# Kernel tuning notes

Hardware: AMD Instinct MI355X
Metric: run time of the kernel (lower is better)

The kernel has to match this reference:

```python
import jax, jax.numpy as jnp
import numpy as np

NORM_EPS = 1e-8   # eps in F.normalize
PDIST_EPS = 1e-6  # eps in nn.PairwiseDistance(2, eps=1e-06): ||x1 - x2 + eps||_2


def setup_inputs() -> dict:
    key = jax.random.key(0)
    student_output = jax.random.normal(key, (16384, 1024), dtype=jnp.float32)
    return {"student_output": student_output}


def reference(student_output) -> jnp.ndarray:
    x = student_output
    n = x.shape[0]
    # --- pairwise NN via inner products on L2-normalized vectors (no-grad in original) ---
    norms = jnp.linalg.norm(x, axis=-1, keepdims=True)
    xn = x / jnp.maximum(norms, NORM_EPS)          # F.normalize(x, p=2, eps=1e-8)
    dots = xn @ xn.T                               # [N, N]
    dots = dots.at[jnp.diag_indices(n)].set(-1.0)  # mask self-similarity
    I = jnp.argmax(dots, axis=1)                   # nearest neighbor indices
    # --- pairwise L2 distance to NN (torch adds eps to the difference) ---
    diff = x - x[I] + PDIST_EPS                    # [N, D]
    distances = jnp.sqrt(jnp.sum(diff * diff, axis=-1))
    loss = -jnp.mean(jnp.log(distances))
    return loss
```

## Files before the change

### kernel.cpp

```cpp
#include <hip/hip_runtime.h>
#include <hip/hip_bf16.h>

#define KN 16384
#define KD 1024
#define NB (KN / 128)

typedef __attribute__((ext_vector_type(4))) int   i32x4;
typedef __attribute__((ext_vector_type(8))) int   i32x8;
typedef __attribute__((ext_vector_type(4))) float f32x4;
typedef __attribute__((ext_vector_type(2))) unsigned int u32x2;

#define SCALE_M6 0x79797979
#define FMT_FP4  4

__device__ __forceinline__ i32x8 ldg_frag4(const unsigned char* p) {
  const i32x4 v = *(const i32x4*)p;
  return __builtin_shufflevector(v, v, 0, 1, 2, 3, -1, -1, -1, -1);
}

#define IDX_MASK 0x3FFFu
#define VAL_MASK 0xFFFFC000u

__device__ __forceinline__ unsigned fp4n(float x) {
  const float a = fabsf(x);
  unsigned c = (unsigned)(a >= 0.25f) + (unsigned)(a >= 0.75f)
             + (unsigned)(a >= 1.25f) + (unsigned)(a >= 1.75f)
             + (unsigned)(a >= 2.5f)  + (unsigned)(a >= 3.5f)
             + (unsigned)(a >= 5.0f);
  return c | ((__float_as_uint(x) >> 28) & 8u);
}

#if defined(__has_builtin)
#if __has_builtin(__builtin_amdgcn_cvt_scalef32_pk_fp4_f32)
#define HW_FP4 1
#endif
#endif

__global__ __launch_bounds__(256) void k_normalize(const float* __restrict__ x,
                                                   unsigned char* __restrict__ xn,
                                                   unsigned* __restrict__ best) {
  const int lane = threadIdx.x & 63;
  const int wave = threadIdx.x >> 6;
  const int row  = (blockIdx.x << 2) + wave;
  if (lane == 0) best[row] = 0u;
  const float4* xr = (const float4*)(x + (size_t)row * KD);
  const float4 v0 = xr[(lane << 2) + 0];
  const float4 v1 = xr[(lane << 2) + 1];
  const float4 v2 = xr[(lane << 2) + 2];
  const float4 v3 = xr[(lane << 2) + 3];
  float ss = v0.x * v0.x + v0.y * v0.y + v0.z * v0.z + v0.w * v0.w
           + v1.x * v1.x + v1.y * v1.y + v1.z * v1.z + v1.w * v1.w
           + v2.x * v2.x + v2.y * v2.y + v2.z * v2.z + v2.w * v2.w
           + v3.x * v3.x + v3.y * v3.y + v3.z * v3.z + v3.w * v3.w;
#pragma unroll
  for (int off = 32; off > 0; off >>= 1) ss += __shfl_xor(ss, off);
  const float scale = 64.0f / fmaxf(sqrtf(ss), 1e-8f);
  const float s0  = v0.x * scale, s1  = v0.y * scale, s2  = v0.z * scale, s3  = v0.w * scale;
  const float s4  = v1.x * scale, s5  = v1.y * scale, s6  = v1.z * scale, s7  = v1.w * scale;
  const float s8  = v2.x * scale, s9  = v2.y * scale, s10 = v2.z * scale, s11 = v2.w * scale;
  const float s12 = v3.x * scale, s13 = v3.y * scale, s14 = v3.z * scale, s15 = v3.w * scale;
  unsigned w0 = 0u, w1 = 0u;
#ifdef HW_FP4
  w0 = __builtin_amdgcn_cvt_scalef32_pk_fp4_f32(w0, s0,  s1,  1.0f, 0);
  w0 = __builtin_amdgcn_cvt_scalef32_pk_fp4_f32(w0, s2,  s3,  1.0f, 1);
  w0 = __builtin_amdgcn_cvt_scalef32_pk_fp4_f32(w0, s4,  s5,  1.0f, 2);
  w0 = __builtin_amdgcn_cvt_scalef32_pk_fp4_f32(w0, s6,  s7,  1.0f, 3);
  w1 = __builtin_amdgcn_cvt_scalef32_pk_fp4_f32(w1, s8,  s9,  1.0f, 0);
  w1 = __builtin_amdgcn_cvt_scalef32_pk_fp4_f32(w1, s10, s11, 1.0f, 1);
  w1 = __builtin_amdgcn_cvt_scalef32_pk_fp4_f32(w1, s12, s13, 1.0f, 2);
  w1 = __builtin_amdgcn_cvt_scalef32_pk_fp4_f32(w1, s14, s15, 1.0f, 3);
#else
  w0 = (fp4n(s0)  | (fp4n(s1)  << 4)) | ((fp4n(s2)  | (fp4n(s3)  << 4)) << 8)
     | ((fp4n(s4) | (fp4n(s5)  << 4)) << 16) | ((fp4n(s6)  | (fp4n(s7)  << 4)) << 24);
  w1 = (fp4n(s8)  | (fp4n(s9)  << 4)) | ((fp4n(s10) | (fp4n(s11) << 4)) << 8)
     | ((fp4n(s12)| (fp4n(s13) << 4)) << 16) | ((fp4n(s14) | (fp4n(s15) << 4)) << 24);
#endif
  unsigned char* base = xn + ((size_t)(row >> 4) << 13) + ((size_t)(lane >> 3) << 10)
                      + ((((lane & 6) << 3) + (row & 15)) << 4) + ((lane & 1) << 3);
  *(u32x2*)base = (u32x2){w0, w1};
}

template <bool DIAG>
__device__ __forceinline__ void epilogue(const f32x4 (&acc)[4][4], int by, int bx,
                                         int wm, int wn, int quad, int l15,
                                         unsigned* __restrict__ best) {
  const int rowbase = (by << 7) + wm * 64 + (quad << 2);
  const int colbase = (bx << 7) + wn * 64 + l15;
  unsigned cm0 = 0u, cm1 = 0u, cm2 = 0u, cm3 = 0u;
#pragma unroll
  for (int i = 0; i < 4; i++) {
#pragma unroll
    for (int r = 0; r < 4; r++) {
      const int grow = rowbase + i * 16 + r;
      const unsigned grx = (unsigned)grow ^ IDX_MASK;
      unsigned rm = 0u;
#pragma unroll
      for (int j = 0; j < 4; j++) {
        const int gcol = colbase + j * 16;
        unsigned t = (__float_as_uint(fmaf(acc[i][j][r], 0.125f, 3.0f)) << 9) & VAL_MASK;
        if (DIAG && gcol == grow) t = 0u;
        const unsigned rc = t | ((unsigned)gcol ^ IDX_MASK);
        const unsigned cc = t | grx;
        rm = rm > rc ? rm : rc;
        if (j == 0) cm0 = cm0 > cc ? cm0 : cc;
        if (j == 1) cm1 = cm1 > cc ? cm1 : cc;
        if (j == 2) cm2 = cm2 > cc ? cm2 : cc;
        if (j == 3) cm3 = cm3 > cc ? cm3 : cc;
      }
#pragma unroll
      for (int off = 1; off < 16; off <<= 1) {
        const unsigned o = __shfl_xor(rm, off);
        rm = rm > o ? rm : o;
      }
      if (l15 == 0) atomicMax(best + grow, rm);
    }
  }
  if (!DIAG) {
    unsigned cm[4] = {cm0, cm1, cm2, cm3};
#pragma unroll
    for (int j = 0; j < 4; j++) {
      unsigned o = __shfl_xor(cm[j], 16);
      cm[j] = cm[j] > o ? cm[j] : o;
      o = __shfl_xor(cm[j], 32);
      cm[j] = cm[j] > o ? cm[j] : o;
      if (quad == 0) atomicMax(best + colbase + j * 16, cm[j]);
    }
  }
}

__global__ __launch_bounds__(256, 2) void k_nn_argmax(const unsigned char* __restrict__ xn,
                                                      unsigned* __restrict__ best) {
  const int id = blockIdx.x;
  int d, by;
  if (id < 8192) {
    const int o   = id & 7;
    const int idp = id >> 3;
    const int k   = idp >> 6;
    const int p   = idp & 63;
    const int q   = o + (k << 3);
    by = ((q & 15) << 3) + (p & 7);
    d  = ((q >> 4) << 3) + (p >> 3);
  } else {
    d  = NB / 2;
    by = id - 8192;
  }
  const int bx = (by + d) & (NB - 1);

  const int tid  = threadIdx.x;
  const int lane = tid & 63;
  const int wave = tid >> 6;
  const int wm   = wave >> 1;
  const int wn   = wave & 1;
  const int quad = lane >> 4;
  const int l15  = lane & 15;

  f32x4 acc[4][4];
#pragma unroll
  for (int i = 0; i < 4; i++)
#pragma unroll
    for (int j = 0; j < 4; j++) acc[i][j] = (f32x4){0.f, 0.f, 0.f, 0.f};

  const unsigned char* pa = xn + ((size_t)((by << 3) + (wm << 2)) << 13) + (lane << 4);
  const unsigned char* pb = xn + ((size_t)((bx << 3) + (wn << 2)) << 13) + (lane << 4);

#pragma unroll 2
  for (int kb = 0; kb < 8; kb++) {
    const int ko = kb << 10;
    const i32x8 a0 = ldg_frag4(pa + ko);
    const i32x8 a1 = ldg_frag4(pa + (1 << 13) + ko);
    const i32x8 a2 = ldg_frag4(pa + (2 << 13) + ko);
    const i32x8 a3 = ldg_frag4(pa + (3 << 13) + ko);
    const i32x8 b0 = ldg_frag4(pb + ko);
    const i32x8 b1 = ldg_frag4(pb + (1 << 13) + ko);
    const i32x8 b2 = ldg_frag4(pb + (2 << 13) + ko);
    const i32x8 b3 = ldg_frag4(pb + (3 << 13) + ko);
    acc[0][0] = __builtin_amdgcn_mfma_scale_f32_16x16x128_f8f6f4(a0, b0, acc[0][0], FMT_FP4, FMT_FP4, 0, SCALE_M6, 0, SCALE_M6);
    acc[1][0] = __builtin_amdgcn_mfma_scale_f32_16x16x128_f8f6f4(a1, b0, acc[1][0], FMT_FP4, FMT_FP4, 0, SCALE_M6, 0, SCALE_M6);
    acc[2][0] = __builtin_amdgcn_mfma_scale_f32_16x16x128_f8f6f4(a2, b0, acc[2][0], FMT_FP4, FMT_FP4, 0, SCALE_M6, 0, SCALE_M6);
    acc[3][0] = __builtin_amdgcn_mfma_scale_f32_16x16x128_f8f6f4(a3, b0, acc[3][0], FMT_FP4, FMT_FP4, 0, SCALE_M6, 0, SCALE_M6);
    acc[0][1] = __builtin_amdgcn_mfma_scale_f32_16x16x128_f8f6f4(a0, b1, acc[0][1], FMT_FP4, FMT_FP4, 0, SCALE_M6, 0, SCALE_M6);
    acc[1][1] = __builtin_amdgcn_mfma_scale_f32_16x16x128_f8f6f4(a1, b1, acc[1][1], FMT_FP4, FMT_FP4, 0, SCALE_M6, 0, SCALE_M6);
    acc[2][1] = __builtin_amdgcn_mfma_scale_f32_16x16x128_f8f6f4(a2, b1, acc[2][1], FMT_FP4, FMT_FP4, 0, SCALE_M6, 0, SCALE_M6);
    acc[3][1] = __builtin_amdgcn_mfma_scale_f32_16x16x128_f8f6f4(a3, b1, acc[3][1], FMT_FP4, FMT_FP4, 0, SCALE_M6, 0, SCALE_M6);
    acc[0][2] = __builtin_amdgcn_mfma_scale_f32_16x16x128_f8f6f4(a0, b2, acc[0][2], FMT_FP4, FMT_FP4, 0, SCALE_M6, 0, SCALE_M6);
    acc[1][2] = __builtin_amdgcn_mfma_scale_f32_16x16x128_f8f6f4(a1, b2, acc[1][2], FMT_FP4, FMT_FP4, 0, SCALE_M6, 0, SCALE_M6);
    acc[2][2] = __builtin_amdgcn_mfma_scale_f32_16x16x128_f8f6f4(a2, b2, acc[2][2], FMT_FP4, FMT_FP4, 0, SCALE_M6, 0, SCALE_M6);
    acc[3][2] = __builtin_amdgcn_mfma_scale_f32_16x16x128_f8f6f4(a3, b2, acc[3][2], FMT_FP4, FMT_FP4, 0, SCALE_M6, 0, SCALE_M6);
    acc[0][3] = __builtin_amdgcn_mfma_scale_f32_16x16x128_f8f6f4(a0, b3, acc[0][3], FMT_FP4, FMT_FP4, 0, SCALE_M6, 0, SCALE_M6);
    acc[1][3] = __builtin_amdgcn_mfma_scale_f32_16x16x128_f8f6f4(a1, b3, acc[1][3], FMT_FP4, FMT_FP4, 0, SCALE_M6, 0, SCALE_M6);
    acc[2][3] = __builtin_amdgcn_mfma_scale_f32_16x16x128_f8f6f4(a2, b3, acc[2][3], FMT_FP4, FMT_FP4, 0, SCALE_M6, 0, SCALE_M6);
    acc[3][3] = __builtin_amdgcn_mfma_scale_f32_16x16x128_f8f6f4(a3, b3, acc[3][3], FMT_FP4, FMT_FP4, 0, SCALE_M6, 0, SCALE_M6);
  }

  if (d == 0) epilogue<true>(acc, by, bx, wm, wn, quad, l15, best);
  else        epilogue<false>(acc, by, bx, wm, wn, quad, l15, best);
}

__global__ __launch_bounds__(256) void k_dist(const float* __restrict__ x,
                                              const unsigned* __restrict__ best,
                                              float* __restrict__ rowlog) {
  const int lane = threadIdx.x & 63;
  const int wave = threadIdx.x >> 6;
  const int row  = (blockIdx.x << 2) + wave;
  const int nb   = (int)((~best[row]) & IDX_MASK);
  const float4* ar = (const float4*)(x + (size_t)row * KD);
  const float4* br = (const float4*)(x + (size_t)nb * KD);
  float ss = 0.f;
#pragma unroll
  for (int q = 0; q < 4; q++) {
    const float4 a = ar[lane + 64 * q];
    const float4 b = br[lane + 64 * q];
    const float dx = a.x - b.x + 1e-6f;
    const float dy = a.y - b.y + 1e-6f;
    const float dz = a.z - b.z + 1e-6f;
    const float dw = a.w - b.w + 1e-6f;
    ss += dx * dx + dy * dy + dz * dz + dw * dw;
  }
#pragma unroll
  for (int off = 32; off > 0; off >>= 1) ss += __shfl_xor(ss, off);
  if (lane == 0) rowlog[row] = -logf(sqrtf(ss));
}

__global__ __launch_bounds__(1024) void k_final(const float* __restrict__ rowlog,
                                                float* __restrict__ out) {
  const int tid = threadIdx.x;
  float s = 0.f;
  for (int i = tid; i < KN; i += 1024) s += rowlog[i];
#pragma unroll
  for (int off = 32; off > 0; off >>= 1) s += __shfl_down(s, off);
  __shared__ float ws[16];
  if ((tid & 63) == 0) ws[tid >> 6] = s;
  __syncthreads();
  if (tid == 0) {
    float t = 0.f;
#pragma unroll
    for (int i = 0; i < 16; i++) t += ws[i];
    out[0] = t / (float)KN;
  }
}

extern "C" void kernel_launch(void* const* d_in, const int* in_sizes, int n_in,
                              void* d_out, int out_size, void* d_ws, size_t ws_size,
                              hipStream_t stream) {
  const float* x = (const float*)d_in[0];
  float* out = (float*)d_out;

  char* ws = (char*)d_ws;
  unsigned char* xn = (unsigned char*)ws;
  unsigned* best = (unsigned*)(ws + (size_t)KN * KD / 2);
  float* rowlog = (float*)(ws + (size_t)KN * KD / 2 + (size_t)KN * 4);

  k_normalize<<<KN / 4, 256, 0, stream>>>(x, xn, best);
  k_nn_argmax<<<8192 + 64, 256, 0, stream>>>(xn, best);
  k_dist<<<KN / 4, 256, 0, stream>>>(x, best, rowlog);
  k_final<<<1, 1024, 0, stream>>>(rowlog, out);
}
```

Before: 221.6 us.

## Switch NN argmax GEMM to 32x32x64 FP4 MFMA with matching epilogue

Replaces the 4x4 grid of 16x16x128 scaled FP4 MFMAs per wave with a 2x2 grid of 32x32x64 MFMAs, remapping lane offsets into the existing packed FP4 layout and iterating 16 K-steps instead of 8. The epilogue is rewritten for the 32x32 accumulator layout, reducing rows across 32 lanes and columns across the two half-waves. The goal is fewer MFMA issues and fragment loads per K step, and fewer atomics per wave. It relies on the new lane-to-address mapping matching the 32x32x64 operand layout exactly.

```diff
diff --git a/kernel.cpp b/kernel.cpp
--- a/kernel.cpp
+++ b/kernel.cpp
@@ -5,10 +5,10 @@
 #define KD 1024
 #define NB (KN / 128)
 
-typedef __attribute__((ext_vector_type(4))) int   i32x4;
-typedef __attribute__((ext_vector_type(8))) int   i32x8;
-typedef __attribute__((ext_vector_type(4))) float f32x4;
-typedef __attribute__((ext_vector_type(2))) unsigned int u32x2;
+typedef __attribute__((ext_vector_type(4)))  int   i32x4;
+typedef __attribute__((ext_vector_type(8)))  int   i32x8;
+typedef __attribute__((ext_vector_type(16))) float f32x16;
+typedef __attribute__((ext_vector_type(2)))  unsigned int u32x2;
 
 #define SCALE_M6 0x79797979
 #define FMT_FP4  4
@@ -81,49 +81,46 @@
 }
 
 template <bool DIAG>
-__device__ __forceinline__ void epilogue(const f32x4 (&acc)[4][4], int by, int bx,
-                                         int wm, int wn, int quad, int l15,
-                                         unsigned* __restrict__ best) {
-  const int rowbase = (by << 7) + wm * 64 + (quad << 2);
-  const int colbase = (bx << 7) + wn * 64 + l15;
-  unsigned cm0 = 0u, cm1 = 0u, cm2 = 0u, cm3 = 0u;
-#pragma unroll
-  for (int i = 0; i < 4; i++) {
-#pragma unroll
-    for (int r = 0; r < 4; r++) {
-      const int grow = rowbase + i * 16 + r;
+__device__ __forceinline__ void epilogue32(const f32x16 (&acc)[2][2], int by, int bx,
+                                           int wm, int wn, int l31, int hi,
+                                           unsigned* __restrict__ best) {
+  const int rowbase = (by << 7) + wm * 64 + (hi << 2);
+  const int colbase = (bx << 7) + wn * 64 + l31;
+  unsigned cm0 = 0u, cm1 = 0u;
+#pragma unroll
+  for (int m = 0; m < 2; m++) {
+#pragma unroll
+    for (int reg = 0; reg < 16; reg++) {
+      const int grow = rowbase + m * 32 + (reg & 3) + ((reg >> 2) << 3);
       const unsigned grx = (unsigned)grow ^ IDX_MASK;
       unsigned rm = 0u;
 #pragma unroll
-      for (int j = 0; j < 4; j++) {
-        const int gcol = colbase + j * 16;
-        unsigned t = (__float_as_uint(fmaf(acc[i][j][r], 0.125f, 3.0f)) << 9) & VAL_MASK;
+      for (int n = 0; n < 2; n++) {
+        const int gcol = colbase + n * 32;
+        unsigned t = (__float_as_uint(fmaf(acc[m][n][reg], 0.125f, 3.0f)) << 9) & VAL_MASK;
         if (DIAG && gcol == grow) t = 0u;
         const unsigned rc = t | ((unsigned)gcol ^ IDX_MASK);
         const unsigned cc = t | grx;
         rm = rm > rc ? rm : rc;
-        if (j == 0) cm0 = cm0 > cc ? cm0 : cc;
-        if (j == 1) cm1 = cm1 > cc ? cm1 : cc;
-        if (j == 2) cm2 = cm2 > cc ? cm2 : cc;
-        if (j == 3) cm3 = cm3 > cc ? cm3 : cc;
+        if (n == 0) cm0 = cm0 > cc ? cm0 : cc;
+        else        cm1 = cm1 > cc ? cm1 : cc;
       }
 #pragma unroll
-      for (int off = 1; off < 16; off <<= 1) {
+      for (int off = 1; off < 32; off <<= 1) {
         const unsigned o = __shfl_xor(rm, off);
         rm = rm > o ? rm : o;
       }
-      if (l15 == 0) atomicMax(best + grow, rm);
+      if (l31 == 0) atomicMax(best + grow, rm);
     }
   }
   if (!DIAG) {
-    unsigned cm[4] = {cm0, cm1, cm2, cm3};
-#pragma unroll
-    for (int j = 0; j < 4; j++) {
-      unsigned o = __shfl_xor(cm[j], 16);
-      cm[j] = cm[j] > o ? cm[j] : o;
-      o = __shfl_xor(cm[j], 32);
-      cm[j] = cm[j] > o ? cm[j] : o;
-      if (quad == 0) atomicMax(best + colbase + j * 16, cm[j]);
+    unsigned o = __shfl_xor(cm0, 32);
+    cm0 = cm0 > o ? cm0 : o;
+    o = __shfl_xor(cm1, 32);
+    cm1 = cm1 > o ? cm1 : o;
+    if (hi == 0) {
+      atomicMax(best + colbase, cm0);
+      atomicMax(best + colbase + 32, cm1);
     }
   }
 }
@@ -151,49 +148,38 @@
   const int wave = tid >> 6;
   const int wm   = wave >> 1;
   const int wn   = wave & 1;
-  const int quad = lane >> 4;
-  const int l15  = lane & 15;
-
-  f32x4 acc[4][4];
-#pragma unroll
-  for (int i = 0; i < 4; i++)
-#pragma unroll
-    for (int j = 0; j < 4; j++) acc[i][j] = (f32x4){0.f, 0.f, 0.f, 0.f};
-
-  const unsigned char* pa = xn + ((size_t)((by << 3) + (wm << 2)) << 13) + (lane << 4);
-  const unsigned char* pb = xn + ((size_t)((bx << 3) + (wn << 2)) << 13) + (lane << 4);
-
-#pragma unroll 2
-  for (int kb = 0; kb < 8; kb++) {
-    const int ko = kb << 10;
-    const i32x8 a0 = ldg_frag4(pa + ko);
-    const i32x8 a1 = ldg_frag4(pa + (1 << 13) + ko);
-    const i32x8 a2 = ldg_frag4(pa + (2 << 13) + ko);
-    const i32x8 a3 = ldg_frag4(pa + (3 << 13) + ko);
-    const i32x8 b0 = ldg_frag4(pb + ko);
-    const i32x8 b1 = ldg_frag4(pb + (1 << 13) + ko);
-    const i32x8 b2 = ldg_frag4(pb + (2 << 13) + ko);
-    const i32x8 b3 = ldg_frag4(pb + (3 << 13) + ko);
-    acc[0][0] = __builtin_amdgcn_mfma_scale_f32_16x16x128_f8f6f4(a0, b0, acc[0][0], FMT_FP4, FMT_FP4, 0, SCALE_M6, 0, SCALE_M6);
-    acc[1][0] = __builtin_amdgcn_mfma_scale_f32_16x16x128_f8f6f4(a1, b0, acc[1][0], FMT_FP4, FMT_FP4, 0, SCALE_M6, 0, SCALE_M6);
-    acc[2][0] = __builtin_amdgcn_mfma_scale_f32_16x16x128_f8f6f4(a2, b0, acc[2][0], FMT_FP4, FMT_FP4, 0, SCALE_M6, 0, SCALE_M6);
-    acc[3][0] = __builtin_amdgcn_mfma_scale_f32_16x16x128_f8f6f4(a3, b0, acc[3][0], FMT_FP4, FMT_FP4, 0, SCALE_M6, 0, SCALE_M6);
-    acc[0][1] = __builtin_amdgcn_mfma_scale_f32_16x16x128_f8f6f4(a0, b1, acc[0][1], FMT_FP4, FMT_FP4, 0, SCALE_M6, 0, SCALE_M6);
-    acc[1][1] = __builtin_amdgcn_mfma_scale_f32_16x16x128_f8f6f4(a1, b1, acc[1][1], FMT_FP4, FMT_FP4, 0, SCALE_M6, 0, SCALE_M6);
-    acc[2][1] = __builtin_amdgcn_mfma_scale_f32_16x16x128_f8f6f4(a2, b1, acc[2][1], FMT_FP4, FMT_FP4, 0, SCALE_M6, 0, SCALE_M6);
-    acc[3][1] = __builtin_amdgcn_mfma_scale_f32_16x16x128_f8f6f4(a3, b1, acc[3][1], FMT_FP4, FMT_FP4, 0, SCALE_M6, 0, SCALE_M6);
-    acc[0][2] = __builtin_amdgcn_mfma_scale_f32_16x16x128_f8f6f4(a0, b2, acc[0][2], FMT_FP4, FMT_FP4, 0, SCALE_M6, 0, SCALE_M6);
-    acc[1][2] = __builtin_amdgcn_mfma_scale_f32_16x16x128_f8f6f4(a1, b2, acc[1][2], FMT_FP4, FMT_FP4, 0, SCALE_M6, 0, SCALE_M6);
-    acc[2][2] = __builtin_amdgcn_mfma_scale_f32_16x16x128_f8f6f4(a2, b2, acc[2][2], FMT_FP4, FMT_FP4, 0, SCALE_M6, 0, SCALE_M6);
-    acc[3][2] = __builtin_amdgcn_mfma_scale_f32_16x16x128_f8f6f4(a3, b2, acc[3][2], FMT_FP4, FMT_FP4, 0, SCALE_M6, 0, SCALE_M6);
-    acc[0][3] = __builtin_amdgcn_mfma_scale_f32_16x16x128_f8f6f4(a0, b3, acc[0][3], FMT_FP4, FMT_FP4, 0, SCALE_M6, 0, SCALE_M6);
-    acc[1][3] = __builtin_amdgcn_mfma_scale_f32_16x16x128_f8f6f4(a1, b3, acc[1][3], FMT_FP4, FMT_FP4, 0, SCALE_M6, 0, SCALE_M6);
-    acc[2][3] = __builtin_amdgcn_mfma_scale_f32_16x16x128_f8f6f4(a2, b3, acc[2][3], FMT_FP4, FMT_FP4, 0, SCALE_M6, 0, SCALE_M6);
-    acc[3][3] = __builtin_amdgcn_mfma_scale_f32_16x16x128_f8f6f4(a3, b3, acc[3][3], FMT_FP4, FMT_FP4, 0, SCALE_M6, 0, SCALE_M6);
-  }
-
-  if (d == 0) epilogue<true>(acc, by, bx, wm, wn, quad, l15, best);
-  else        epilogue<false>(acc, by, bx, wm, wn, quad, l15, best);
+  const int l31  = lane & 31;
+  const int hi   = lane >> 5;
+
+  f32x16 acc[2][2];
+#pragma unroll
+  for (int m = 0; m < 2; m++)
+#pragma unroll
+    for (int n = 0; n < 2; n++)
+#pragma unroll
+      for (int r = 0; r < 16; r++) acc[m][n][r] = 0.f;
+
+  const int lofs = (((lane >> 4) & 1) << 13) + (hi << 8) + ((lane & 15) << 4);
+  const unsigned char* pa0 = xn + ((size_t)((by << 3) + (wm << 2)) << 13) + lofs;
+  const unsigned char* pa1 = pa0 + 16384;
+  const unsigned char* pb0 = xn + ((size_t)((bx << 3) + (wn << 2)) << 13) + lofs;
+  const unsigned char* pb1 = pb0 + 16384;
+
+#pragma unroll 4
+  for (int ks = 0; ks < 16; ks++) {
+    const int ko = ks << 9;
+    const i32x8 a0 = ldg_frag4(pa0 + ko);
+    const i32x8 a1 = ldg_frag4(pa1 + ko);
+    const i32x8 b0 = ldg_frag4(pb0 + ko);
+    const i32x8 b1 = ldg_frag4(pb1 + ko);
+    acc[0][0] = __builtin_amdgcn_mfma_scale_f32_32x32x64_f8f6f4(a0, b0, acc[0][0], FMT_FP4, FMT_FP4, 0, SCALE_M6, 0, SCALE_M6);
+    acc[1][0] = __builtin_amdgcn_mfma_scale_f32_32x32x64_f8f6f4(a1, b0, acc[1][0], FMT_FP4, FMT_FP4, 0, SCALE_M6, 0, SCALE_M6);
+    acc[0][1] = __builtin_amdgcn_mfma_scale_f32_32x32x64_f8f6f4(a0, b1, acc[0][1], FMT_FP4, FMT_FP4, 0, SCALE_M6, 0, SCALE_M6);
+    acc[1][1] = __builtin_amdgcn_mfma_scale_f32_32x32x64_f8f6f4(a1, b1, acc[1][1], FMT_FP4, FMT_FP4, 0, SCALE_M6, 0, SCALE_M6);
+  }
+
+  if (d == 0) epilogue32<true>(acc, by, bx, wm, wn, l31, hi, best);
+  else        epilogue32<false>(acc, by, bx, wm, wn, l31, hi, best);
 }
 
 __global__ __launch_bounds__(256) void k_dist(const float* __restrict__ x,
```

Measured after the change: 268.7 us. 1.21x slower.
